# Optimization experiments

Measured on AMD Instinct MI355X. Metric: run time of the kernel, lower is better.

Reference implementation:

```python
import jax, jax.numpy as jnp
from jax import lax
import numpy as np

DN = ('NCHW', 'OIHW', 'NCHW')

def conv(x, w, b, stride, pad):
    y = lax.conv_general_dilated(x, w, (stride, stride), [(pad, pad), (pad, pad)], dimension_numbers=DN)
    return y + b[None, :, None, None]

def conv_t(x, w, b):
    # torch ConvTranspose2d(k=4, s=2, p=1); w is torch layout [Cin, Cout, 4, 4]
    wf = jnp.flip(w, (2, 3)).transpose(1, 0, 2, 3)  # -> OIHW
    y = lax.conv_general_dilated(x, wf, (1, 1), [(2, 2), (2, 2)], lhs_dilation=(2, 2), dimension_numbers=DN)
    return y + b[None, :, None, None]

def setup_inputs() -> dict:
    key = jax.random.key(0)
    ks = jax.random.split(key, 20)
    B, C_in, H, W = 8, 1, 512, 512
    hid, zc, K = 64, 64, 512
    s = 0.05
    inp = {
        'x': jax.random.uniform(ks[0], (B, C_in, H, W), jnp.float32),
        # encoder: three 4x4 s2 convs + one 3x3 s1 conv
        'enc_w1': jax.random.normal(ks[1], (hid, C_in, 4, 4), jnp.float32) * s,
        'enc_b1': jnp.zeros((hid,), jnp.float32),
        'enc_w2': jax.random.normal(ks[2], (hid, hid, 4, 4), jnp.float32) * s,
        'enc_b2': jnp.zeros((hid,), jnp.float32),
        'enc_w3': jax.random.normal(ks[3], (hid, hid, 4, 4), jnp.float32) * s,
        'enc_b3': jnp.zeros((hid,), jnp.float32),
        'enc_w4': jax.random.normal(ks[4], (zc, hid, 3, 3), jnp.float32) * s,
        'enc_b4': jnp.zeros((zc,), jnp.float32),
        # codebook, uniform(-1/K, 1/K) as in torch init
        'codebook': jax.random.uniform(ks[5], (K, zc), jnp.float32, -1.0 / K, 1.0 / K),
        # decoder: 3x3 s1 conv + three 4x4 s2 conv-transposes (torch [Cin,Cout,kH,kW] layout)
        'dec_w1': jax.random.normal(ks[6], (hid, zc, 3, 3), jnp.float32) * s,
        'dec_b1': jnp.zeros((hid,), jnp.float32),
        'dec_tw1': jax.random.normal(ks[7], (hid, hid, 4, 4), jnp.float32) * s,
        'dec_tb1': jnp.zeros((hid,), jnp.float32),
        'dec_tw2': jax.random.normal(ks[8], (hid, hid, 4, 4), jnp.float32) * s,
        'dec_tb2': jnp.zeros((hid,), jnp.float32),
        'dec_tw3': jax.random.normal(ks[9], (hid, C_in, 4, 4), jnp.float32) * s,
        'dec_tb3': jnp.zeros((C_in,), jnp.float32),
    }
    return inp

def _forward(x, enc_w1, enc_b1, enc_w2, enc_b2, enc_w3, enc_b3, enc_w4, enc_b4,
             codebook, dec_w1, dec_b1, dec_tw1, dec_tb1, dec_tw2, dec_tb2, dec_tw3, dec_tb3):
    # ---- encoder ----
    h = jax.nn.relu(conv(x, enc_w1, enc_b1, 2, 1))
    h = jax.nn.relu(conv(h, enc_w2, enc_b2, 2, 1))
    h = jax.nn.relu(conv(h, enc_w3, enc_b3, 2, 1))
    z = conv(h, enc_w4, enc_b4, 1, 1)  # [B, zc, H/8, W/8]
    # ---- vector quantizer ----
    B, C, Hh, Ww = z.shape
    z_flat = z.transpose(0, 2, 3, 1).reshape(-1, C)  # [N, C]
    dist = (jnp.sum(z_flat ** 2, axis=1, keepdims=True)
            + jnp.sum(codebook ** 2, axis=1)
            - 2.0 * z_flat @ codebook.T)  # [N, K]
    idx = jnp.argmin(dist, axis=1)
    z_q = codebook[idx].reshape(B, Hh, Ww, C).transpose(0, 3, 1, 2)
    sg = lax.stop_gradient
    vq_loss = jnp.mean((sg(z_q) - z) ** 2) + 0.25 * jnp.mean((z_q - sg(z)) ** 2)
    z_q = z + sg(z_q - z)  # straight-through
    # ---- decoder ----
    d = jax.nn.relu(conv(z_q, dec_w1, dec_b1, 1, 1))
    d = jax.nn.relu(conv_t(d, dec_tw1, dec_tb1))
    d = jax.nn.relu(conv_t(d, dec_tw2, dec_tb2))
    x_hat = jax.nn.sigmoid(conv_t(d, dec_tw3, dec_tb3))
    return x_hat, vq_loss

def reference(x, enc_w1, enc_b1, enc_w2, enc_b2, enc_w3, enc_b3, enc_w4, enc_b4,
              codebook, dec_w1, dec_b1, dec_tw1, dec_tb1, dec_tw2, dec_tb2, dec_tw3, dec_tb3):
    return _forward(x, enc_w1, enc_b1, enc_w2, enc_b2, enc_w3, enc_b3, enc_w4, enc_b4,
                    codebook, dec_w1, dec_b1, dec_tw1, dec_tb1, dec_tw2, dec_tb2, dec_tw3, dec_tb3)
```

## Files before the change

kernel.cpp:

```cpp
#include <hip/hip_runtime.h>
#include <math.h>


typedef __bf16 bf16x8_t __attribute__((ext_vector_type(8)));
typedef _Float16 f16x8_t __attribute__((ext_vector_type(8)));
typedef float f32x4_t __attribute__((ext_vector_type(4)));
typedef _Float16 h2_t __attribute__((ext_vector_type(2)));

union FragU { uint4 u; bf16x8_t b; };
union Frag16 { uint4 u; f16x8_t h; };

__device__ inline f32x4_t mfma16(bf16x8_t a, bf16x8_t b, f32x4_t c) {
    return __builtin_amdgcn_mfma_f32_16x16x32_bf16(a, b, c, 0, 0, 0);
}
__device__ inline f32x4_t mfma16h(f16x8_t a, f16x8_t b, f32x4_t c) {
    return __builtin_amdgcn_mfma_f32_16x16x32_f16(a, b, c, 0, 0, 0);
}

__device__ inline void gl_lds16(const void* g, void* l) {
    __builtin_amdgcn_global_load_lds((const __attribute__((address_space(1))) void*)g,
                                     (__attribute__((address_space(3))) void*)l, 16, 0, 0);
}

__device__ inline unsigned bf16rne(float f) {
    unsigned u = __float_as_uint(f);
    u += 0x7FFFu + ((u >> 16) & 1u);
    return u >> 16;
}
__device__ inline unsigned pack2(float lo, float hi) {
    return bf16rne(lo) | (bf16rne(hi) << 16);
}
__device__ inline unsigned pack2h(float lo, float hi) {
    union { h2_t h; unsigned u; } r;
    r.h[0] = (_Float16)lo; r.h[1] = (_Float16)hi;
    return r.u;
}
__device__ inline unsigned short f16bits(float v) {
    union { _Float16 h; unsigned short s; } x; x.h = (_Float16)v; return x.s;
}
__device__ inline float f16lo(unsigned u) {
    union { unsigned u; h2_t h; } x; x.u = u; return (float)x.h[0];
}
__device__ inline float f16hi(unsigned u) {
    union { unsigned u; h2_t h; } x; x.u = u; return (float)x.h[1];
}
__device__ inline float bl(unsigned u) { return __uint_as_float(u << 16); }
__device__ inline float bh(unsigned u) { return __uint_as_float(u & 0xffff0000u); }

#if defined(__has_builtin)
#if __has_builtin(__builtin_amdgcn_fdot2)
#define HAS_FDOT2 1
#endif
#endif

__device__ inline float dot2h(unsigned x, unsigned w, float a) {
#ifdef HAS_FDOT2
    union { unsigned u; h2_t h; } ax, bw;
    ax.u = x; bw.u = w;
    return __builtin_amdgcn_fdot2(ax.h, bw.h, a, false);
#else
    union { unsigned u; _Float16 h[2]; } ax, bw;
    ax.u = x; bw.u = w;
    a = fmaf((float)ax.h[0], (float)bw.h[0], a);
    return fmaf((float)ax.h[1], (float)bw.h[1], a);
#endif
}
__device__ inline float dot8(uint4 x, uint4 w, float a) {
    a = dot2h(x.x, w.x, a); a = dot2h(x.y, w.y, a);
    a = dot2h(x.z, w.z, a); a = dot2h(x.w, w.w, a);
    return a;
}

template<int NR, int KW_, int SW, int CIC, int SPT, int NT, int OUTM, int DBUF>
__global__ __launch_bounds__(256) void conv_mfma(
    const unsigned short* __restrict__ in, const unsigned short* __restrict__ wp,
    const float* __restrict__ bias, void* __restrict__ outp,
    int Hp, int Wp, int PS, int nchunks, int Cout, int ncog,
    int Hpo, int Wpo, int relu)
{
    constexpr int W_ST = SW * (SPT - 1) + KW_;
    constexpr int SLOTS_PP = CIC / 8;
    constexpr int ROW_SLOTS = W_ST * SLOTS_PP;
    constexpr int SEGS = (ROW_SLOTS + 63) / 64;
    constexpr int KT = NR * KW_;
    constexpr int CSTEPS = CIC / 32;
    constexpr int BUFSZ = NR * W_ST * CIC;
    __shared__ __align__(16) unsigned short sh[(DBUF ? 2 : 1) * BUFSZ];

    int t = threadIdx.x, lane = t & 63, wv = t >> 6;
    int bx = blockIdx.x;
    int owt, khalf;
    if constexpr (OUTM == 4) { khalf = bx; owt = 0; }
    else { khalf = 0; owt = bx; }
    int ch0 = khalf * nchunks;
    int ohg = blockIdx.y;
    int bz = blockIdx.z; int nb = bz / ncog; int cog = bz % ncog;
    int ow0 = owt * SPT;
    int row0 = SW * ohg;
    int col0 = SW * ow0;
    int coh = wv & 1;
    int sph = wv >> 1;
    int m = lane & 15, g = lane >> 4;

    f32x4_t acc[2][NT];
#pragma unroll
    for (int a = 0; a < 2; ++a)
#pragma unroll
        for (int u2 = 0; u2 < NT; ++u2) acc[a][u2] = (f32x4_t){0.f, 0.f, 0.f, 0.f};

    auto stage = [&](int ch, unsigned short* buf) {
        for (int u_ = wv; u_ < NR * SEGS; u_ += 4) {
            int r = u_ / SEGS, seg = u_ - r * SEGS;
            int slot = seg * 64 + lane;
            int p = slot / SLOTS_PP;
            int uu = slot & (SLOTS_PP - 1);
            if (p < W_ST) {
                int su = (uu - (p & 7)) & (SLOTS_PP - 1);
                const unsigned short* gsrc = in +
                    (((size_t)nb * Hp + (row0 + r)) * Wp + (col0 + p)) * PS + (ch0 + ch) * CIC + su * 8;
                unsigned short* ldst = buf + ((size_t)(r * ROW_SLOTS + seg * 64 + lane)) * 8;
                gl_lds16(gsrc, ldst);
            }
        }
    };

    auto compute = [&](int ch, const unsigned short* buf) {
        int sbase = (ch0 + ch) * (KT * CSTEPS);
#pragma unroll
        for (int tap = 0; tap < KT; ++tap) {
            const int r_l = tap / KW_, kwp = tap % KW_;
#pragma unroll
            for (int cs = 0; cs < CSTEPS; ++cs) {
                int s = sbase + tap * CSTEPS + cs;
                const uint4* wr = (const uint4*)wp + (size_t)(s * 4 + g) * Cout + cog * 64 + coh * 32 + m;
                FragU a0, a1;
                a0.u = wr[0];
                a1.u = wr[16];
#pragma unroll
                for (int u2 = 0; u2 < NT; ++u2) {
                    int sp_l = sph * (SPT / 2) + u2 * 16 + m;
                    int p = SW * sp_l + kwp;
                    int off = (cs * 32 + g * 8 + ((p & 7) << 3)) & (CIC - 1);
                    FragU bb;
                    bb.u = *(const uint4*)(buf + (size_t)(r_l * W_ST + p) * CIC + off);
                    acc[0][u2] = mfma16(a0.b, bb.b, acc[0][u2]);
                    acc[1][u2] = mfma16(a1.b, bb.b, acc[1][u2]);
                }
            }
        }
    };

    stage(0, sh);
    __syncthreads();
    for (int ch = 0; ch < nchunks; ++ch) {
        if constexpr (DBUF != 0) {
            if (ch + 1 < nchunks) stage(ch + 1, sh + (size_t)((ch + 1) & 1) * BUFSZ);
        }
        compute(ch, DBUF ? (sh + (size_t)(ch & 1) * BUFSZ) : sh);
        if (ch + 1 < nchunks) {
            if constexpr (DBUF == 0) {
                __syncthreads();
                stage(ch + 1, sh);
            }
            __syncthreads();
        }
    }
    if constexpr (OUTM == 4) {
        float* ob = (float*)outp;
#pragma unroll
        for (int a = 0; a < 2; ++a) {
#pragma unroll
            for (int u2 = 0; u2 < NT; ++u2) {
                int ow = ow0 + sph * (SPT / 2) + u2 * 16 + m;
                float4 st = {acc[a][u2][0], acc[a][u2][1], acc[a][u2][2], acc[a][u2][3]};
                *(float4*)(ob + ((((size_t)khalf * 8 + nb) * 4096 + ohg * 64 + ow) * 64
                          + (coh * 32 + a * 16 + g * 4))) = st;
            }
        }
    } else {
#pragma unroll
        for (int a = 0; a < 2; ++a) {
            int co = cog * 64 + coh * 32 + a * 16 + g * 4;
            float4 bv = *(const float4*)(bias + co);
#pragma unroll
            for (int u2 = 0; u2 < NT; ++u2) {
                int ow = ow0 + sph * (SPT / 2) + u2 * 16 + m;
                float v0 = acc[a][u2][0] + bv.x;
                float v1 = acc[a][u2][1] + bv.y;
                float v2 = acc[a][u2][2] + bv.z;
                float v3 = acc[a][u2][3] + bv.w;
                if (relu) {
                    v0 = fmaxf(v0, 0.f); v1 = fmaxf(v1, 0.f);
                    v2 = fmaxf(v2, 0.f); v3 = fmaxf(v3, 0.f);
                }
                unsigned short* ob = (unsigned short*)outp;
                uint2 st;
                if constexpr (OUTM == 3) st = (uint2){pack2h(v0, v1), pack2h(v2, v3)};
                else                     st = (uint2){pack2(v0, v1), pack2(v2, v3)};
                *(uint2*)(ob + (((size_t)nb * Hpo + ohg + 1) * Wpo + (ow + 1)) * 64
                          + (coh * 32 + a * 16 + g * 4)) = st;
            }
        }
    }
}

__global__ __launch_bounds__(256) void k_dec1red(const float* __restrict__ pf,
    const float* __restrict__ bias, unsigned short* __restrict__ d1)
{
    int idx = blockIdx.x * 256 + threadIdx.x;
    int c8 = idx & 7;
    int rest = idx >> 3;
    int pix = rest & 4095, n = rest >> 12;
    const float* p0 = pf + (size_t)rest * 64 + c8 * 8;
    const float* p1 = p0 + (size_t)32768 * 64;
    float4 a0 = *(const float4*)p0, a1 = *(const float4*)(p0 + 4);
    float4 b0 = *(const float4*)p1, b1 = *(const float4*)(p1 + 4);
    float4 s0 = *(const float4*)(bias + c8 * 8);
    float4 s1 = *(const float4*)(bias + c8 * 8 + 4);
    float v0 = fmaxf(a0.x + b0.x + s0.x, 0.f);
    float v1 = fmaxf(a0.y + b0.y + s0.y, 0.f);
    float v2 = fmaxf(a0.z + b0.z + s0.z, 0.f);
    float v3 = fmaxf(a0.w + b0.w + s0.w, 0.f);
    float v4 = fmaxf(a1.x + b1.x + s1.x, 0.f);
    float v5 = fmaxf(a1.y + b1.y + s1.y, 0.f);
    float v6 = fmaxf(a1.z + b1.z + s1.z, 0.f);
    float v7 = fmaxf(a1.w + b1.w + s1.w, 0.f);
    uint4 st = {pack2(v0, v1), pack2(v2, v3), pack2(v4, v5), pack2(v6, v7)};
    int h = pix >> 6, w = pix & 63;
    *(uint4*)(d1 + ((size_t)(n * 66 + h + 1) * 66 + (w + 1)) * 64 + c8 * 8) = st;
}

__global__ __launch_bounds__(256) void k_enc2w(
    const unsigned short* __restrict__ in, const unsigned short* __restrict__ wp,
    const float* __restrict__ bias, unsigned short* __restrict__ out)
{
    __shared__ __align__(16) unsigned short sh[16512];
    int t = threadIdx.x, lane = t & 63, wv = t >> 6;
    int m = lane & 15, g = lane >> 4;
    int ohg = blockIdx.x, n = blockIdx.y;

    f32x4_t acc[4][2];
#pragma unroll
    for (int a = 0; a < 4; ++a)
#pragma unroll
        for (int u2 = 0; u2 < 2; ++u2) acc[a][u2] = (f32x4_t){0.f, 0.f, 0.f, 0.f};

    const uint4* wp4 = (const uint4*)wp;
#pragma unroll
    for (int kh = 0; kh < 4; ++kh) {
        if (kh) __syncthreads();
        const unsigned short* rowp = in + ((size_t)(n * 258 + 2 * ohg + kh) * 258) * 64;
        for (int q = t; q < 2064; q += 256) {
            int p = q >> 3, uu = q & 7;
            int su = (uu - ((p >> 1) & 7)) & 7;
            gl_lds16(rowp + (size_t)p * 64 + su * 8, sh + (size_t)q * 8);
        }
        __syncthreads();
#pragma unroll
        for (int kwp = 0; kwp < 4; ++kwp) {
#pragma unroll
            for (int cs = 0; cs < 2; ++cs) {
                int s = (kh * 4 + kwp) * 2 + cs;
                const uint4* wr = wp4 + (size_t)(s * 4 + g) * 64 + m;
                FragU A[4];
#pragma unroll
                for (int a = 0; a < 4; ++a) A[a].u = wr[a * 16];
#pragma unroll
                for (int u2 = 0; u2 < 2; ++u2) {
                    int sp_l = wv * 32 + u2 * 16 + m;
                    int p = 2 * sp_l + kwp;
                    int rot = (sp_l + (kwp >> 1)) & 7;
                    int off = (cs * 32 + g * 8 + rot * 8) & 63;
                    FragU B;
                    B.u = *(const uint4*)(sh + (size_t)p * 64 + off);
#pragma unroll
                    for (int a = 0; a < 4; ++a)
                        acc[a][u2] = mfma16(A[a].b, B.b, acc[a][u2]);
                }
            }
        }
    }
#pragma unroll
    for (int a = 0; a < 4; ++a) {
        float4 bv = *(const float4*)(bias + a * 16 + g * 4);
#pragma unroll
        for (int u2 = 0; u2 < 2; ++u2) {
            int ow = wv * 32 + u2 * 16 + m;
            float v0 = fmaxf(acc[a][u2][0] + bv.x, 0.f);
            float v1 = fmaxf(acc[a][u2][1] + bv.y, 0.f);
            float v2 = fmaxf(acc[a][u2][2] + bv.z, 0.f);
            float v3 = fmaxf(acc[a][u2][3] + bv.w, 0.f);
            uint2 st = {pack2(v0, v1), pack2(v2, v3)};
            *(uint2*)(out + ((size_t)(n * 130 + ohg + 1) * 130 + ow + 1) * 64
                      + a * 16 + g * 4) = st;
        }
    }
}

template<int OUTM>
__global__ __launch_bounds__(256) void k_convtf(
    const unsigned short* __restrict__ in, const unsigned short* __restrict__ wp,
    const float* __restrict__ bias, unsigned short* __restrict__ out,
    int Hpi, int Wpi, int Hpo, int Wpo)
{
    __shared__ __align__(16) unsigned short sh[8704];
    int t = threadIdx.x, lane = t & 63, wv = t >> 6;
    int m = lane & 15, g = lane >> 4;
    int pw = wv & 1, u2h = wv >> 1;
    int owt = blockIdx.x;
    int by = blockIdx.y; int ohg = by >> 1, ph = by & 1;
    int n = blockIdx.z;
    int col0 = owt * 64;

    const unsigned short* an = in + ((size_t)(n * Hpi + ohg + ph) * Wpi + col0) * 64;
    for (int q = t; q < 1056; q += 256) {
        int r = q / 528, rest = q - r * 528;
        int p = rest >> 3, uu = rest & 7;
        int su = (uu - (p & 7)) & 7;
        gl_lds16(an + ((size_t)r * Wpi + p) * 64 + su * 8, sh + (size_t)q * 8);
    }
    f32x4_t acc[4][2];
#pragma unroll
    for (int a = 0; a < 4; ++a)
#pragma unroll
        for (int u2i = 0; u2i < 2; ++u2i) acc[a][u2i] = (f32x4_t){0.f, 0.f, 0.f, 0.f};
    __syncthreads();

    const uint4* ws4 = (const uint4*)(wp + (size_t)(ph * 2 + pw) * 16384);
#pragma unroll
    for (int jh = 0; jh < 2; ++jh) {
#pragma unroll
        for (int jw = 0; jw < 2; ++jw) {
#pragma unroll
            for (int cs = 0; cs < 2; ++cs) {
                int s = (jh * 2 + jw) * 2 + cs;
                const uint4* wr = ws4 + (size_t)(s * 4 + g) * 64 + m;
                FragU A[4];
#pragma unroll
                for (int a = 0; a < 4; ++a) A[a].u = wr[a * 16];
#pragma unroll
                for (int u2i = 0; u2i < 2; ++u2i) {
                    int u2 = u2h * 2 + u2i;
                    int p = u2 * 16 + m + pw + jw;
                    int off = (cs * 32 + g * 8 + ((p & 7) << 3)) & 63;
                    FragU B;
                    B.u = *(const uint4*)(sh + (size_t)(jh * 528 + p * 8) * 8 + off);
#pragma unroll
                    for (int a = 0; a < 4; ++a)
                        acc[a][u2i] = mfma16(A[a].b, B.b, acc[a][u2i]);
                }
            }
        }
    }
    unsigned pk[4][2][2];
#pragma unroll
    for (int a = 0; a < 4; ++a) {
        float4 bv = *(const float4*)(bias + a * 16 + g * 4);
#pragma unroll
        for (int u2i = 0; u2i < 2; ++u2i) {
            float v0 = fmaxf(acc[a][u2i][0] + bv.x, 0.f);
            float v1 = fmaxf(acc[a][u2i][1] + bv.y, 0.f);
            float v2 = fmaxf(acc[a][u2i][2] + bv.z, 0.f);
            float v3 = fmaxf(acc[a][u2i][3] + bv.w, 0.f);
            if constexpr (OUTM == 3) { pk[a][u2i][0] = pack2h(v0, v1); pk[a][u2i][1] = pack2h(v2, v3); }
            else                     { pk[a][u2i][0] = pack2(v0, v1);  pk[a][u2i][1] = pack2(v2, v3); }
        }
    }
    __syncthreads();
#pragma unroll
    for (int u2i = 0; u2i < 2; ++u2i) {
        int u2 = u2h * 2 + u2i;
        int lp = 2 * (u2 * 16 + m) + pw;
#pragma unroll
        for (int a = 0; a < 4; ++a)
            *(uint2*)(sh + (size_t)lp * 68 + a * 16 + g * 4) =
                (uint2){pk[a][u2i][0], pk[a][u2i][1]};
    }
    __syncthreads();
    unsigned short* gbase = out + ((size_t)(n * Hpo + 2 * ohg + ph + 1) * Wpo
                          + 2 * col0 + 1) * 64;
#pragma unroll
    for (int i = 0; i < 4; ++i) {
        int s = i * 256 + t;
        int p = s >> 3, c8 = s & 7;
        uint4 v = *(const uint4*)(sh + (size_t)p * 68 + c8 * 8);
        *(uint4*)(gbase + (size_t)s * 8) = v;
    }
}

__global__ __launch_bounds__(256) void k_enc4(
    const unsigned short* __restrict__ a3, const unsigned short* __restrict__ wp,
    const float* __restrict__ bias, unsigned short* __restrict__ zH,
    unsigned short* __restrict__ zL)
{
    __shared__ __align__(16) unsigned short sh[16896];
    int t = threadIdx.x, lane = t & 63, wv = t >> 6;
    int wc = wv & 1, wr = wv >> 1;
    int m = lane & 15, g = lane >> 4;
    int L = blockIdx.x;
    int xcd = L & 7, j = L >> 3;
    int cog = j & 3;
    int rt = (j >> 2) + xcd * 32;
    int row0 = rt * 128;
    int n = row0 >> 12;
    int oh0 = (row0 & 4095) >> 6;

    const unsigned short* an = a3 + ((size_t)(n * 66 + oh0) * 66) * 64;
    for (int seg = wv; seg < 33; seg += 4) {
        int slot = seg * 64 + lane;
        if (slot < 2112) {
            int r = slot / 528, rest = slot - r * 528;
            int p = rest >> 3, uu = rest & 7;
            int su = (uu - p) & 7;
            gl_lds16(an + ((size_t)(r * 66 + p)) * 64 + su * 8, sh + (size_t)slot * 8);
        }
    }
    f32x4_t acc[4][4];
#pragma unroll
    for (int a = 0; a < 4; ++a)
#pragma unroll
        for (int b = 0; b < 4; ++b) acc[a][b] = (f32x4_t){0.f, 0.f, 0.f, 0.f};
    __syncthreads();

#pragma unroll
    for (int tap = 0; tap < 9; ++tap) {
        const int kh = tap / 3, kwp = tap % 3;
#pragma unroll
        for (int cs = 0; cs < 2; ++cs) {
            int s = tap * 2 + cs;
            const uint4* wr4 = (const uint4*)wp + (size_t)(s * 4 + g) * 512 + cog * 128 + wc * 64 + m;
            FragU A[4];
#pragma unroll
            for (int ci = 0; ci < 4; ++ci) A[ci].u = wr4[ci * 16];
#pragma unroll
            for (int si = 0; si < 4; ++si) {
                int sp_l = wr * 64 + si * 16 + m;
                int r_l = (sp_l >> 6) + kh;
                int px = (sp_l & 63) + kwp;
                int off = (cs * 4 + g + px) & 7;
                FragU B;
                B.u = *(const uint4*)(sh + ((size_t)(r_l * 528 + px * 8 + off)) * 8);
#pragma unroll
                for (int ci = 0; ci < 4; ++ci)
                    acc[ci][si] = mfma16(A[ci].b, B.b, acc[ci][si]);
            }
        }
    }
    float4 bv[4];
#pragma unroll
    for (int ci = 0; ci < 4; ++ci)
        bv[ci] = *(const float4*)(bias + cog * 128 + wc * 64 + ci * 16 + g * 4);

    __syncthreads();
#pragma unroll
    for (int ci = 0; ci < 4; ++ci) {
#pragma unroll
        for (int si = 0; si < 4; ++si) {
            float v0 = acc[ci][si][0] + bv[ci].x;
            float v1 = acc[ci][si][1] + bv[ci].y;
            float v2 = acc[ci][si][2] + bv[ci].z;
            float v3 = acc[ci][si][3] + bv[ci].w;
            unsigned h0 = pack2h(v0, v1);
            unsigned h1 = pack2h(v2, v3);
            int row = wr * 64 + si * 16 + m;
            int col = wc * 64 + ci * 16 + g * 4;
            *(uint2*)(sh + (size_t)row * 132 + col) = (uint2){h0, h1};
        }
    }
    __syncthreads();
#pragma unroll
    for (int i = 0; i < 8; ++i) {
        int idx = i * 256 + t;
        int row = idx >> 4, c16 = idx & 15;
        uint4 v = *(const uint4*)(sh + (size_t)row * 132 + c16 * 8);
        int col = cog * 128 + c16 * 8;
        int sblk = col >> 5, off = col & 31;
        *(uint4*)(zH + ((size_t)sblk * 32768 + row0 + row) * 32 + off) = v;
    }
    __syncthreads();
#pragma unroll
    for (int ci = 0; ci < 4; ++ci) {
#pragma unroll
        for (int si = 0; si < 4; ++si) {
            float v0 = acc[ci][si][0] + bv[ci].x;
            float v1 = acc[ci][si][1] + bv[ci].y;
            float v2 = acc[ci][si][2] + bv[ci].z;
            float v3 = acc[ci][si][3] + bv[ci].w;
            unsigned h0 = pack2h(v0, v1);
            unsigned h1 = pack2h(v2, v3);
            unsigned l0 = pack2h(v0 - f16lo(h0), v1 - f16hi(h0));
            unsigned l1 = pack2h(v2 - f16lo(h1), v3 - f16hi(h1));
            int row = wr * 64 + si * 16 + m;
            int col = wc * 64 + ci * 16 + g * 4;
            *(uint2*)(sh + (size_t)row * 132 + col) = (uint2){l0, l1};
        }
    }
    __syncthreads();
#pragma unroll
    for (int i = 0; i < 8; ++i) {
        int idx = i * 256 + t;
        int row = idx >> 4, c16 = idx & 15;
        uint4 v = *(const uint4*)(sh + (size_t)row * 132 + c16 * 8);
        int col = cog * 128 + c16 * 8;
        int sblk = col >> 5, off = col & 31;
        *(uint4*)(zL + ((size_t)sblk * 32768 + row0 + row) * 32 + off) = v;
    }
}

__global__ __launch_bounds__(256) void k_halo_all(
    unsigned short* a1, unsigned short* a2, unsigned short* a3,
    unsigned short* zq, unsigned short* d1)
{
    unsigned short* buf; int Hp, Wp, PS;
    switch (blockIdx.z) {
        case 0: buf = a1; Hp = 258; Wp = 258; PS = 64; break;
        case 1: buf = a2; Hp = 130; Wp = 130; PS = 64; break;
        case 2: buf = a3; Hp = 66; Wp = 66; PS = 64; break;
        case 3: buf = zq; Hp = 66; Wp = 66; PS = 512; break;
        default: buf = d1; Hp = 66; Wp = 66; PS = 64; break;
    }
    int per = 2 * Wp + 2 * (Hp - 2);
    int chunks = PS >> 3;
    int total = per * chunks;
    int n = blockIdx.y;
    for (int i = blockIdx.x * 256 + threadIdx.x; i < total; i += gridDim.x * 256) {
        int pix = i / chunks, c = i - pix * chunks;
        int h, w;
        if (pix < Wp) { h = 0; w = pix; }
        else if (pix < 2 * Wp) { h = Hp - 1; w = pix - Wp; }
        else { int q = pix - 2 * Wp; h = 1 + (q >> 1); w = (q & 1) ? (Wp - 1) : 0; }
        uint4 zz = {0, 0, 0, 0};
        *(uint4*)(buf + (((size_t)n * Hp + h) * Wp + w) * PS + c * 8) = zz;
    }
}

__device__ inline void prep_conv_dev(const float* __restrict__ w,
    unsigned short* __restrict__ o, int Cout, int Cin, int T, int CIC, int idx)
{
    if (idx >= Cout * Cin * T) return;
    int tap = idx % T; int r = idx / T; int ci = r % Cin; int co = r / Cin;
    int chunk = ci / CIC, cil = ci % CIC;
    int k = chunk * (T * CIC) + tap * CIC + cil;
    int s = k >> 5, g = (k >> 3) & 3, j = k & 7;
    o[((size_t)(s * 4 + g) * Cout + co) * 8 + j] = (unsigned short)bf16rne(w[idx]);
}

__device__ inline void prep_wT_dev(const float* __restrict__ w,
    unsigned short* __restrict__ o, int idx)
{
    if (idx >= 65536) return;
    int ci = idx & 63; int r = idx >> 6;
    int jw = r & 1; r >>= 1;
    int jh = r & 1; r >>= 1;
    int co = r & 63; r >>= 6;
    int pw = r & 1; int ph = (r >> 1) & 1;
    int kh = (1 - ph) + 2 * (1 - jh);
    int kw = (1 - pw) + 2 * (1 - jw);
    int k = (jh * 2 + jw) * 64 + ci;
    int s = k >> 5, g = (k >> 3) & 3, j = k & 7;
    o[(size_t)(ph * 2 + pw) * 16384 + ((size_t)(s * 4 + g) * 64 + co) * 8 + j] =
        (unsigned short)bf16rne(w[((ci * 64 + co) * 4 + kh) * 4 + kw]);
}

__global__ __launch_bounds__(256) void k_prep_all(
    const float* __restrict__ enc_w2, const float* __restrict__ enc_w3,
    const float* __restrict__ enc_w4, const float* __restrict__ dec_w1,
    const float* __restrict__ tw1, const float* __restrict__ tw2,
    const float* __restrict__ cb,
    unsigned short* __restrict__ wA2, unsigned short* __restrict__ wA3,
    unsigned short* __restrict__ wB1, unsigned short* __restrict__ wB2,
    unsigned short* __restrict__ wC1, unsigned short* __restrict__ wC2,
    unsigned short* __restrict__ cbF,
    float* __restrict__ cn2)
{
    int idx = blockIdx.x * 256 + threadIdx.x;
    switch (blockIdx.y) {
    case 0: prep_conv_dev(enc_w2, wA2, 64, 64, 16, 64, idx); break;
    case 1: prep_conv_dev(enc_w3, wA3, 64, 64, 16, 64, idx); break;
    case 2: prep_conv_dev(enc_w4, wB1, 512, 64, 9, 64, idx); break;
    case 3: prep_conv_dev(dec_w1, wB2, 64, 512, 9, 64, idx); break;
    case 4: prep_wT_dev(tw1, wC1, idx); break;
    case 5: prep_wT_dev(tw2, wC2, idx); break;
    case 6: {
        if (idx < 262144) {
            int c = idx & 511, k = idx >> 9;
            int cblk = k >> 7, kl = k & 127, s = c >> 5, g = (c >> 3) & 3, j = c & 7;
            size_t off = ((((size_t)cblk * 16 + s) * 4 + g) * 128 + kl) * 8 + j;
            cbF[off] = f16bits(cb[idx]);
        }
    } break;
    default: {
        int code = blockIdx.x * 4 + (threadIdx.x >> 6);
        if (code < 512) {
            int l = threadIdx.x & 63;
            float s = 0.f;
#pragma unroll
            for (int i = 0; i < 8; ++i) {
                float v = cb[code * 512 + l + i * 64];
                s = fmaf(v, v, s);
            }
#pragma unroll
            for (int off = 32; off > 0; off >>= 1) s += __shfl_xor(s, off);
            if (l == 0) cn2[code] = 0.5f * s;
        }
    } break;
    }
}

__global__ __launch_bounds__(256) void k_conv1(const float* __restrict__ x,
    const float* __restrict__ w, const float* __restrict__ b, unsigned short* __restrict__ out)
{
    __shared__ __align__(16) unsigned short sh[128 * 132];
    int t = threadIdx.x;
    int oh = blockIdx.x;
    int n = blockIdx.y;
    int ow = t;
    const float* xn = x + (size_t)n * 262144;
    float xv[16];
#pragma unroll
    for (int kh = 0; kh < 4; ++kh) {
        int ih = 2 * oh - 1 + kh;
        bool rok = (unsigned)ih < 512u;
        int ihc = min(max(ih, 0), 511);
#pragma unroll
        for (int kw = 0; kw < 4; ++kw) {
            int iw = 2 * ow - 1 + kw;
            bool ok = rok && ((unsigned)iw < 512u);
            int iwc = min(max(iw, 0), 511);
            float v = xn[ihc * 512 + iwc];
            xv[kh * 4 + kw] = ok ? v : 0.f;
        }
    }
    unsigned uo[32];
#pragma unroll
    for (int co2 = 0; co2 < 32; ++co2) {
        float a0 = b[2 * co2], a1 = b[2 * co2 + 1];
#pragma unroll
        for (int q = 0; q < 16; ++q) {
            a0 = fmaf(xv[q], w[(2 * co2) * 16 + q], a0);
            a1 = fmaf(xv[q], w[(2 * co2 + 1) * 16 + q], a1);
        }
        uo[co2] = pack2(fmaxf(a0, 0.f), fmaxf(a1, 0.f));
    }
    unsigned short* rowbase = out + (((size_t)n * 258 + oh + 1) * 258 + 1) * 64;
#pragma unroll
    for (int pass = 0; pass < 2; ++pass) {
        if (pass) __syncthreads();
        if ((t >> 7) == pass) {
            int p = t & 127;
            unsigned short* rowp = sh + (size_t)p * 132;
#pragma unroll
            for (int i = 0; i < 8; ++i) {
                uint4 st = {uo[4 * i], uo[4 * i + 1], uo[4 * i + 2], uo[4 * i + 3]};
                *(uint4*)(rowp + i * 8) = st;
            }
        }
        __syncthreads();
        unsigned short* gbase = rowbase + (size_t)pass * 8192;
#pragma unroll
        for (int i = 0; i < 4; ++i) {
            int s = i * 256 + t;
            int p = s >> 3, c = s & 7;
            uint4 v = *(const uint4*)(sh + (size_t)p * 132 + c * 8);
            *(uint4*)(gbase + (size_t)s * 8) = v;
        }
    }
}

__device__ inline bool better_sc(float av, int ai, float bv, int bi) {
    return av > bv || (av == bv && ai < bi);
}

__global__ __launch_bounds__(256) void k_vqgemm(
    const unsigned short* __restrict__ zH, const unsigned short* __restrict__ cbF,
    const float* __restrict__ cn2, int* __restrict__ candI)
{
    __shared__ __align__(16) unsigned short shA[20480];
    int t = threadIdx.x, lane = t & 63, wv = t >> 6;
    int wc = wv & 1, wr = wv >> 1;
    int m = lane & 15, g = lane >> 4;
    int L = blockIdx.x;
    int xcd = L & 7, kk = L >> 3;
    int cblk = kk & 3;
    int row0 = ((kk >> 2) + xcd * 32) * 128;

    f32x4_t acc[4][4];
#pragma unroll
    for (int a = 0; a < 4; ++a)
#pragma unroll
        for (int b = 0; b < 4; ++b) acc[a][b] = (f32x4_t){0.f, 0.f, 0.f, 0.f};

    const uint4* bF = (const uint4*)cbF + (size_t)cblk * 8192;

    auto stage = [&](int c, int bi) {
        unsigned short* dst = shA + (size_t)bi * 10240;
        for (int q = t; q < 1280; q += 256) {
            int ss = q / 640, rest = q - ss * 640;
            int r = rest / 5, seg = rest - r * 5;
            int s = c * 2 + ss;
            gl_lds16(zH + ((size_t)s * 32768 + row0 + r) * 32 + (seg & 3) * 8,
                     dst + (size_t)q * 8);
        }
    };

    stage(0, 0);
    __syncthreads();
    for (int c = 0; c < 8; ++c) {
        if (c + 1 < 8) stage(c + 1, (c + 1) & 1);
        const unsigned short* buf = shA + (size_t)(c & 1) * 10240;
#pragma unroll
        for (int ss = 0; ss < 2; ++ss) {
            int s = c * 2 + ss;
            Frag16 B[4];
#pragma unroll
            for (int ni = 0; ni < 4; ++ni)
                B[ni].u = bF[(s * 4 + g) * 128 + wc * 64 + ni * 16 + m];
#pragma unroll
            for (int mi = 0; mi < 4; ++mi) {
                Frag16 A;
                A.u = *(const uint4*)(buf + (size_t)(ss * 5120 + (wr * 64 + mi * 16 + m) * 40 + g * 8));
#pragma unroll
                for (int ni = 0; ni < 4; ++ni)
                    acc[mi][ni] = mfma16h(A.h, B[ni].h, acc[mi][ni]);
            }
        }
        if (c + 1 < 8) __syncthreads();
    }
    float* tV = (float*)shA;
    int*   tI = (int*)(shA + 2048);
    float c2v[4];
#pragma unroll
    for (int ni = 0; ni < 4; ++ni) c2v[ni] = cn2[cblk * 128 + wc * 64 + ni * 16 + m];
    int ixb = cblk * 128 + wc * 64 + m;
#pragma unroll
    for (int mi = 0; mi < 4; ++mi) {
#pragma unroll
        for (int r = 0; r < 4; ++r) {
            float a0 = acc[mi][0][r] - c2v[0];
            float a1 = acc[mi][1][r] - c2v[1];
            float a2 = acc[mi][2][r] - c2v[2];
            float a3 = acc[mi][3][r] - c2v[3];
            bool cA = a1 > a0;
            float p1 = cA ? a1 : a0; int pi1 = cA ? ixb + 16 : ixb;
            float p2 = cA ? a0 : a1; int pi2 = cA ? ixb : ixb + 16;
            bool cB = a3 > a2;
            float q1 = cB ? a3 : a2; int qi1 = cB ? ixb + 48 : ixb + 32;
            float q2 = cB ? a2 : a3; int qi2 = cB ? ixb + 32 : ixb + 48;
            bool cC = q1 > p1;
            float v1 = cC ? q1 : p1; int i1 = cC ? qi1 : pi1;
            float sa = cC ? p1 : q1; int sai = cC ? pi1 : qi1;
            float sb = cC ? q2 : p2; int sbi = cC ? qi2 : pi2;
            bool cD = sb > sa;
            float v2 = cD ? sb : sa; int i2 = cD ? sbi : sai;
#pragma unroll
            for (int off = 1; off < 16; off <<= 1) {
                float o1 = __shfl_xor(v1, off); int oi1 = __shfl_xor(i1, off);
                float o2 = __shfl_xor(v2, off); int oi2 = __shfl_xor(i2, off);
                bool c = o1 > v1;
                float w2 = c ? v1 : v2; int w2i = c ? i1 : i2;
                float u2 = c ? o2 : o1; int u2i = c ? oi2 : oi1;
                v1 = c ? o1 : v1; i1 = c ? oi1 : i1;
                bool cc = u2 > w2;
                v2 = cc ? u2 : w2; i2 = cc ? u2i : w2i;
            }
            if (m == 0) {
                int row = wr * 64 + mi * 16 + g * 4 + r;
                tV[(wc * 128 + row) * 2 + 0] = v1; tI[(wc * 128 + row) * 2 + 0] = i1;
                tV[(wc * 128 + row) * 2 + 1] = v2; tI[(wc * 128 + row) * 2 + 1] = i2;
            }
        }
    }
    __syncthreads();
    if (t < 128) {
        float v1 = tV[t * 2], v2 = tV[t * 2 + 1];
        int i1 = tI[t * 2], i2 = tI[t * 2 + 1];
        float o1 = tV[(128 + t) * 2], o2 = tV[(128 + t) * 2 + 1];
        int oi1 = tI[(128 + t) * 2], oi2 = tI[(128 + t) * 2 + 1];
        bool c = o1 > v1;
        float w2 = c ? v1 : v2; int w2i = c ? i1 : i2;
        float u2 = c ? o2 : o1; int u2i = c ? oi2 : oi1;
        v1 = c ? o1 : v1; i1 = c ? oi1 : i1;
        bool cc = u2 > w2;
        v2 = cc ? u2 : w2; i2 = cc ? u2i : w2i;
        candI[((size_t)cblk * 2 + 0) * 32768 + row0 + t] = i1;
        candI[((size_t)cblk * 2 + 1) * 32768 + row0 + t] = i2;
    }
}

__global__ __launch_bounds__(256) void k_vqfinal(
    const unsigned short* __restrict__ zH, const unsigned short* __restrict__ zL,
    const float* __restrict__ cb, const int* __restrict__ candI,
    unsigned short* __restrict__ zq, float* __restrict__ mind)
{
    int t = threadIdx.x, lane = t & 63, wv = t >> 6;
    int row = blockIdx.x * 4 + wv;
    size_t zoff = ((size_t)(lane >> 2) * 32768 + row) * 32 + (lane & 3) * 8;
    uint4 hu = *(const uint4*)(zH + zoff);
    uint4 lu = *(const uint4*)(zL + zoff);
    float z0 = f16lo(hu.x) + f16lo(lu.x);
    float z1 = f16hi(hu.x) + f16hi(lu.x);
    float z2 = f16lo(hu.y) + f16lo(lu.y);
    float z3 = f16hi(hu.y) + f16hi(lu.y);
    float z4 = f16lo(hu.z) + f16lo(lu.z);
    float z5 = f16hi(hu.z) + f16hi(lu.z);
    float z6 = f16lo(hu.w) + f16lo(lu.w);
    float z7 = f16hi(hu.w) + f16hi(lu.w);
    int mycand = (lane < 8) ? candI[(size_t)lane * 32768 + row] : 0;
    int cands[8];
    float d[8];
#pragma unroll
    for (int s = 0; s < 8; ++s) cands[s] = __shfl(mycand, s);
#pragma unroll
    for (int s = 0; s < 8; ++s) {
        const float* cr = cb + (size_t)cands[s] * 512 + lane * 8;
        float4 c0 = *(const float4*)cr;
        float4 c1 = *(const float4*)(cr + 4);
        float e, dd = 0.f;
        e = z0 - c0.x; dd = fmaf(e, e, dd);
        e = z1 - c0.y; dd = fmaf(e, e, dd);
        e = z2 - c0.z; dd = fmaf(e, e, dd);
        e = z3 - c0.w; dd = fmaf(e, e, dd);
        e = z4 - c1.x; dd = fmaf(e, e, dd);
        e = z5 - c1.y; dd = fmaf(e, e, dd);
        e = z6 - c1.z; dd = fmaf(e, e, dd);
        e = z7 - c1.w; dd = fmaf(e, e, dd);
        d[s] = dd;
    }
#pragma unroll
    for (int off = 1; off < 64; off <<= 1) {
#pragma unroll
        for (int s = 0; s < 8; ++s) d[s] += __shfl_xor(d[s], off);
    }
    float bd = d[0]; int bi_ = cands[0];
#pragma unroll
    for (int s = 1; s < 8; ++s) {
        if (d[s] < bd || (d[s] == bd && cands[s] < bi_)) { bd = d[s]; bi_ = cands[s]; }
    }
    {
        int n = row >> 12, hw = row & 4095, h = hw >> 6, w = hw & 63;
        const float* src = cb + (size_t)bi_ * 512 + lane * 8;
        float4 v0 = *(const float4*)src, v1 = *(const float4*)(src + 4);
        uint4 st = {pack2(v0.x, v0.y), pack2(v0.z, v0.w),
                    pack2(v1.x, v1.y), pack2(v1.z, v1.w)};
        *(uint4*)(zq + (((size_t)n * 66 + h + 1) * 66 + (w + 1)) * 512 + lane * 8) = st;
    }
    if (lane == 0) mind[row] = bd;
}

__global__ __launch_bounds__(256, 4) void k_convt_final2(const unsigned short* __restrict__ xp,
    const float* __restrict__ w, const float* __restrict__ b, float* __restrict__ out)
{
    __shared__ __align__(16) unsigned short shx[3 * 1040 * 8];
    __shared__ __align__(16) unsigned wp[16][32];
    int t = threadIdx.x, lane = t & 63, wv = t >> 6;
    int bx = blockIdx.x, q = blockIdx.y, n = blockIdx.z;
    int colbase = bx * 128;
#pragma unroll
    for (int i = 0; i < 2; ++i) {
        int qq = t + i * 256;
        int tap = qq >> 5, c2 = qq & 31;
        wp[tap][c2] = pack2h(w[(2 * c2) * 16 + tap], w[(2 * c2 + 1) * 16 + tap]);
    }
    const unsigned short* an = xp + (size_t)n * 258 * 258 * 64;
    for (int u_ = wv; u_ < 51; u_ += 4) {
        int r = u_ / 17, seg = u_ % 17;
        int slot = seg * 64 + lane;
        if (slot < 1040) {
            int p = slot >> 3, uu = slot & 7;
            int su = (uu - p) & 7;
            int row = min(2 * q + r, 257);
            const unsigned short* gsrc = an + ((size_t)row * 258 + colbase + p) * 64 + su * 8;
            gl_lds16(gsrc, shx + ((size_t)(r * 1040 + slot)) * 8);
        }
    }
    __syncthreads();
    int ow = bx * 256 + t;
    int kwA = (ow + 1) & 1;
    int cA = ((ow + 1) >> 1) + 1 - colbase;
    int cB = cA - 1;
    float b0 = b[0];
    float acc0 = b0, acc1 = b0, acc2 = b0, acc3 = b0;
#pragma unroll 2
    for (int c8 = 0; c8 < 8; ++c8) {
        uint4 xr[3][2];
#pragma unroll
        for (int r = 0; r < 3; ++r) {
            xr[r][0] = *(const uint4*)(shx + (size_t)(r * 1040 + cB * 8 + ((c8 + cB) & 7)) * 8);
            xr[r][1] = *(const uint4*)(shx + (size_t)(r * 1040 + cA * 8 + ((c8 + cA) & 7)) * 8);
        }
        uint4 wA[4], wB[4];
#pragma unroll
        for (int kh = 0; kh < 4; ++kh) {
            wA[kh] = *(const uint4*)&wp[kh * 4 + kwA][c8 * 4];
            wB[kh] = *(const uint4*)&wp[kh * 4 + kwA + 2][c8 * 4];
        }
        acc0 = dot8(xr[1][1], wA[0], acc0); acc0 = dot8(xr[1][0], wB[0], acc0);
        acc0 = dot8(xr[0][1], wA[2], acc0); acc0 = dot8(xr[0][0], wB[2], acc0);
        acc1 = dot8(xr[1][1], wA[1], acc1); acc1 = dot8(xr[1][0], wB[1], acc1);
        acc1 = dot8(xr[0][1], wA[3], acc1); acc1 = dot8(xr[0][0], wB[3], acc1);
        acc2 = dot8(xr[2][1], wA[0], acc2); acc2 = dot8(xr[2][0], wB[0], acc2);
        acc2 = dot8(xr[1][1], wA[2], acc2); acc2 = dot8(xr[1][0], wB[2], acc2);
        acc3 = dot8(xr[2][1], wA[1], acc3); acc3 = dot8(xr[2][0], wB[1], acc3);
        acc3 = dot8(xr[1][1], wA[3], acc3); acc3 = dot8(xr[1][0], wB[3], acc3);
    }
    float accs[4] = {acc0, acc1, acc2, acc3};
    float* on = out + (size_t)n * 262144;
#pragma unroll
    for (int ro = 0; ro < 4; ++ro) {
        int oh = 4 * q - 1 + ro;
        if ((unsigned)oh < 512u)
            on[(size_t)oh * 512 + ow] = 1.0f / (1.0f + __expf(-accs[ro]));
    }
}

__global__ __launch_bounds__(256) void k_loss_final(const float* __restrict__ mind,
    float* __restrict__ out)
{
    __shared__ float redd[4];
    int t = threadIdx.x;
    float s = 0.f;
#pragma unroll 4
    for (int i = 0; i < 32; ++i) {
        float4 v = *(const float4*)(mind + i * 1024 + t * 4);
        s += v.x + v.y + v.z + v.w;
    }
#pragma unroll
    for (int off = 1; off < 64; off <<= 1) s += __shfl_xor(s, off);
    if ((t & 63) == 0) redd[t >> 6] = s;
    __syncthreads();
    if (t == 0)
        out[0] = 1.25f * (redd[0] + redd[1] + redd[2] + redd[3]) * (1.0f / 16777216.0f);
}

extern "C" void kernel_launch(void* const* d_in, const int* in_sizes, int n_in,
                              void* d_out, int out_size, void* d_ws, size_t ws_size,
                              hipStream_t stream)
{
    const float* x      = (const float*)d_in[0];
    const float* enc_w1 = (const float*)d_in[1];
    const float* enc_b1 = (const float*)d_in[2];
    const float* enc_w2 = (const float*)d_in[3];
    const float* enc_b2 = (const float*)d_in[4];
    const float* enc_w3 = (const float*)d_in[5];
    const float* enc_b3 = (const float*)d_in[6];
    const float* enc_w4 = (const float*)d_in[7];
    const float* enc_b4 = (const float*)d_in[8];
    const float* cb     = (const float*)d_in[9];
    const float* dec_w1 = (const float*)d_in[10];
    const float* dec_b1 = (const float*)d_in[11];
    const float* tw1    = (const float*)d_in[12];
    const float* tb1    = (const float*)d_in[13];
    const float* tw2    = (const float*)d_in[14];
    const float* tb2    = (const float*)d_in[15];
    const float* tw3    = (const float*)d_in[16];
    const float* tb3    = (const float*)d_in[17];
    float* out = (float*)d_out;

    unsigned short* a1 = (unsigned short*)d_ws;
    unsigned short* a2 = a1 + 34076672;
    unsigned short* a3 = a2 + 8652800;
    unsigned short* zH = a3 + 2230272;
    unsigned short* zL = zH + 16777216;
    unsigned short* zq = zL + 16777216;
    unsigned short* d1 = zq + 17842176;
    unsigned short* wA2 = d1 + 2230272;
    unsigned short* wA3 = wA2 + 65536;
    unsigned short* wB1 = wA3 + 65536;
    unsigned short* wB2 = wB1 + 294912;
    unsigned short* wC1 = wB2 + 294912;
    unsigned short* wC2 = wC1 + 65536;
    unsigned short* cbF = wC2 + 65536;
    float* cn2 = (float*)(cbF + 262144);
    int*   candI = (int*)(cn2 + 512);
    float* mind = (float*)(candI + 262144);
    float* pf = (float*)zH;

    k_halo_all<<<dim3(65, 8, 5), 256, 0, stream>>>(a1, a2, a3, zq, d1);
    k_prep_all<<<dim3(1152, 8), 256, 0, stream>>>(
        enc_w2, enc_w3, enc_w4, dec_w1, tw1, tw2, cb,
        wA2, wA3, wB1, wB2, wC1, wC2, cbF, cn2);

    k_conv1<<<dim3(256, 8), 256, 0, stream>>>(x, enc_w1, enc_b1, a1);
    k_enc2w<<<dim3(128, 8), 256, 0, stream>>>(a1, wA2, enc_b2, a2);
    conv_mfma<4, 4, 2, 64, 32, 1, 0, 0><<<dim3(2, 64, 8), 256, 0, stream>>>(
        a2, wA3, enc_b3, a3, 130, 130, 64, 1, 64, 1, 66, 66, 1);
    k_enc4<<<1024, 256, 0, stream>>>(a3, wB1, enc_b4, zH, zL);
    k_vqgemm<<<1024, 256, 0, stream>>>(zH, cbF, cn2, candI);
    k_vqfinal<<<8192, 256, 0, stream>>>(zH, zL, cb, candI, zq, mind);
    conv_mfma<3, 3, 1, 64, 64, 2, 4, 0><<<dim3(2, 64, 8), 256, 0, stream>>>(
        zq, wB2, dec_b1, pf, 66, 66, 512, 4, 64, 1, 66, 66, 0);
    k_dec1red<<<1024, 256, 0, stream>>>(pf, dec_b1, d1);
    k_convtf<0><<<dim3(1, 128, 8), 256, 0, stream>>>(d1, wC1, tb1, a2, 66, 66, 130, 130);
    k_convtf<3><<<dim3(2, 256, 8), 256, 0, stream>>>(a2, wC2, tb2, a1, 130, 130, 258, 258);
    k_convt_final2<<<dim3(2, 129, 8), 256, 0, stream>>>(a1, tw3, tb3, out);
    k_loss_final<<<1, 256, 0, stream>>>(mind, out + 2097152);
}
```

Measured before the change: 385.4 us.

## Gather codebook rows by index in decoder conv instead of materializing z_q

The VQ final kernel now writes only the chosen code index per pixel, not a full 512-channel bf16 z_q tensor. The first decoder conv gathers codebook rows (pre-converted to bf16, with a zero row at index 512 for padding halos) directly through the index map while staging to LDS. This removes a roughly 35 MB write and the matching halo zeroing, in exchange for an extra indirect index load per staged pixel. Repeated codebook rows may also hit in cache.

Result: no change. 379.5 us (-1.5%).

```diff
diff --git a/kernel.cpp b/kernel.cpp
--- a/kernel.cpp
+++ b/kernel.cpp
@@ -76,7 +76,7 @@
     const unsigned short* __restrict__ in, const unsigned short* __restrict__ wp,
     const float* __restrict__ bias, void* __restrict__ outp,
     int Hp, int Wp, int PS, int nchunks, int Cout, int ncog,
-    int Hpo, int Wpo, int relu)
+    int Hpo, int Wpo, int relu, const int* __restrict__ idxb)
 {
     constexpr int W_ST = SW * (SPT - 1) + KW_;
     constexpr int SLOTS_PP = CIC / 8;
@@ -90,7 +90,7 @@
     int t = threadIdx.x, lane = t & 63, wv = t >> 6;
     int bx = blockIdx.x;
     int owt, khalf;
-    if constexpr (OUTM == 4) { khalf = bx; owt = 0; }
+    if constexpr (OUTM >= 4) { khalf = bx; owt = 0; }
     else { khalf = 0; owt = bx; }
     int ch0 = khalf * nchunks;
     int ohg = blockIdx.y;
@@ -116,8 +116,14 @@
             int uu = slot & (SLOTS_PP - 1);
             if (p < W_ST) {
                 int su = (uu - (p & 7)) & (SLOTS_PP - 1);
-                const unsigned short* gsrc = in +
-                    (((size_t)nb * Hp + (row0 + r)) * Wp + (col0 + p)) * PS + (ch0 + ch) * CIC + su * 8;
+                const unsigned short* gsrc;
+                if constexpr (OUTM == 5) {
+                    int code = idxb[((size_t)nb * Hp + (row0 + r)) * Wp + (col0 + p)];
+                    gsrc = in + (size_t)code * 512 + (ch0 + ch) * CIC + su * 8;
+                } else {
+                    gsrc = in +
+                        (((size_t)nb * Hp + (row0 + r)) * Wp + (col0 + p)) * PS + (ch0 + ch) * CIC + su * 8;
+                }
                 unsigned short* ldst = buf + ((size_t)(r * ROW_SLOTS + seg * 64 + lane)) * 8;
                 gl_lds16(gsrc, ldst);
             }
@@ -165,7 +171,7 @@
             __syncthreads();
         }
     }
-    if constexpr (OUTM == 4) {
+    if constexpr (OUTM >= 4) {
         float* ob = (float*)outp;
 #pragma unroll
         for (int a = 0; a < 2; ++a) {
@@ -509,14 +515,25 @@
 
 __global__ __launch_bounds__(256) void k_halo_all(
     unsigned short* a1, unsigned short* a2, unsigned short* a3,
-    unsigned short* zq, unsigned short* d1)
-{
+    int* idxb, unsigned short* d1)
+{
+    if (blockIdx.z == 3) {
+        int n = blockIdx.y;
+        int per = 2 * 66 + 2 * 64;
+        for (int i = blockIdx.x * 256 + threadIdx.x; i < per; i += gridDim.x * 256) {
+            int h, w;
+            if (i < 66) { h = 0; w = i; }
+            else if (i < 132) { h = 65; w = i - 66; }
+            else { int q = i - 132; h = 1 + (q >> 1); w = (q & 1) ? 65 : 0; }
+            idxb[((size_t)n * 66 + h) * 66 + w] = 512;
+        }
+        return;
+    }
     unsigned short* buf; int Hp, Wp, PS;
     switch (blockIdx.z) {
         case 0: buf = a1; Hp = 258; Wp = 258; PS = 64; break;
         case 1: buf = a2; Hp = 130; Wp = 130; PS = 64; break;
         case 2: buf = a3; Hp = 66; Wp = 66; PS = 64; break;
-        case 3: buf = zq; Hp = 66; Wp = 66; PS = 512; break;
         default: buf = d1; Hp = 66; Wp = 66; PS = 64; break;
     }
     int per = 2 * Wp + 2 * (Hp - 2);
@@ -570,7 +587,7 @@
     unsigned short* __restrict__ wA2, unsigned short* __restrict__ wA3,
     unsigned short* __restrict__ wB1, unsigned short* __restrict__ wB2,
     unsigned short* __restrict__ wC1, unsigned short* __restrict__ wC2,
-    unsigned short* __restrict__ cbF,
+    unsigned short* __restrict__ cbF, unsigned short* __restrict__ cbB,
     float* __restrict__ cn2)
 {
     int idx = blockIdx.x * 256 + threadIdx.x;
@@ -588,6 +605,10 @@
             size_t off = ((((size_t)cblk * 16 + s) * 4 + g) * 128 + kl) * 8 + j;
             cbF[off] = f16bits(cb[idx]);
         }
+    } break;
+    case 7: {
+        if (idx < 262144) cbB[idx] = (unsigned short)bf16rne(cb[idx]);
+        else if (idx < 262656) cbB[idx] = 0;
     } break;
     default: {
         int code = blockIdx.x * 4 + (threadIdx.x >> 6);
@@ -790,7 +811,7 @@
 __global__ __launch_bounds__(256) void k_vqfinal(
     const unsigned short* __restrict__ zH, const unsigned short* __restrict__ zL,
     const float* __restrict__ cb, const int* __restrict__ candI,
-    unsigned short* __restrict__ zq, float* __restrict__ mind)
+    int* __restrict__ idxb, float* __restrict__ mind)
 {
     int t = threadIdx.x, lane = t & 63, wv = t >> 6;
     int row = blockIdx.x * 4 + wv;
@@ -836,15 +857,11 @@
     for (int s = 1; s < 8; ++s) {
         if (d[s] < bd || (d[s] == bd && cands[s] < bi_)) { bd = d[s]; bi_ = cands[s]; }
     }
-    {
+    if (lane == 0) {
         int n = row >> 12, hw = row & 4095, h = hw >> 6, w = hw & 63;
-        const float* src = cb + (size_t)bi_ * 512 + lane * 8;
-        float4 v0 = *(const float4*)src, v1 = *(const float4*)(src + 4);
-        uint4 st = {pack2(v0.x, v0.y), pack2(v0.z, v0.w),
-                    pack2(v1.x, v1.y), pack2(v1.z, v1.w)};
-        *(uint4*)(zq + (((size_t)n * 66 + h + 1) * 66 + (w + 1)) * 512 + lane * 8) = st;
-    }
-    if (lane == 0) mind[row] = bd;
+        idxb[((size_t)(n * 66 + h + 1)) * 66 + (w + 1)] = bi_;
+        mind[row] = bd;
+    }
 }
 
 __global__ __launch_bounds__(256, 4) void k_convt_final2(const unsigned short* __restrict__ xp,
@@ -961,8 +978,8 @@
     unsigned short* a3 = a2 + 8652800;
     unsigned short* zH = a3 + 2230272;
     unsigned short* zL = zH + 16777216;
-    unsigned short* zq = zL + 16777216;
-    unsigned short* d1 = zq + 17842176;
+    unsigned short* zqr = zL + 16777216;
+    unsigned short* d1 = zqr + 17842176;
     unsigned short* wA2 = d1 + 2230272;
     unsigned short* wA3 = wA2 + 65536;
     unsigned short* wB1 = wA3 + 65536;
@@ -973,22 +990,24 @@
     float* cn2 = (float*)(cbF + 262144);
     int*   candI = (int*)(cn2 + 512);
     float* mind = (float*)(candI + 262144);
+    int*   idxb = (int*)zqr;
+    unsigned short* cbB = zqr + 2 * 34848;
     float* pf = (float*)zH;
 
-    k_halo_all<<<dim3(65, 8, 5), 256, 0, stream>>>(a1, a2, a3, zq, d1);
-    k_prep_all<<<dim3(1152, 8), 256, 0, stream>>>(
+    k_halo_all<<<dim3(65, 8, 5), 256, 0, stream>>>(a1, a2, a3, idxb, d1);
+    k_prep_all<<<dim3(1152, 9), 256, 0, stream>>>(
         enc_w2, enc_w3, enc_w4, dec_w1, tw1, tw2, cb,
-        wA2, wA3, wB1, wB2, wC1, wC2, cbF, cn2);
+        wA2, wA3, wB1, wB2, wC1, wC2, cbF, cbB, cn2);
 
     k_conv1<<<dim3(256, 8), 256, 0, stream>>>(x, enc_w1, enc_b1, a1);
     k_enc2w<<<dim3(128, 8), 256, 0, stream>>>(a1, wA2, enc_b2, a2);
     conv_mfma<4, 4, 2, 64, 32, 1, 0, 0><<<dim3(2, 64, 8), 256, 0, stream>>>(
-        a2, wA3, enc_b3, a3, 130, 130, 64, 1, 64, 1, 66, 66, 1);
+        a2, wA3, enc_b3, a3, 130, 130, 64, 1, 64, 1, 66, 66, 1, nullptr);
     k_enc4<<<1024, 256, 0, stream>>>(a3, wB1, enc_b4, zH, zL);
     k_vqgemm<<<1024, 256, 0, stream>>>(zH, cbF, cn2, candI);
-    k_vqfinal<<<8192, 256, 0, stream>>>(zH, zL, cb, candI, zq, mind);
-    conv_mfma<3, 3, 1, 64, 64, 2, 4, 0><<<dim3(2, 64, 8), 256, 0, stream>>>(
-        zq, wB2, dec_b1, pf, 66, 66, 512, 4, 64, 1, 66, 66, 0);
+    k_vqfinal<<<8192, 256, 0, stream>>>(zH, zL, cb, candI, idxb, mind);
+    conv_mfma<3, 3, 1, 64, 64, 2, 5, 0><<<dim3(2, 64, 8), 256, 0, stream>>>(
+        cbB, wB2, dec_b1, pf, 66, 66, 512, 4, 64, 1, 66, 66, 0, idxb);
     k_dec1red<<<1024, 256, 0, stream>>>(pf, dec_b1, d1);
     k_convtf<0><<<dim3(1, 128, 8), 256, 0, stream>>>(d1, wC1, tb1, a2, 66, 66, 130, 130);
     k_convtf<3><<<dim3(2, 256, 8), 256, 0, stream>>>(a2, wC2, tb2, a1, 130, 130, 258, 258);
```
